# Optimization experiments

Hardware: AMD Instinct MI355X
Metric: run time of the kernel (lower is better)

## Reference

```python
import jax, jax.numpy as jnp
import numpy as np

B, T, D, R = 8, 4096, 768, 16
DB = D // 3  # bucket size (d_img = d_sym = 256, d_rf = D - 2*DB = 256)


def setup_inputs() -> dict:
    key = jax.random.key(0)
    ks = jax.random.split(key, 10)
    s = 0.05
    x = jax.random.normal(ks[0], (B, T, D), dtype=jnp.float32)
    # torch nn.Linear stores weight as (out, in); y = x @ W.T + b
    V_w = jax.random.normal(ks[1], (R, D), dtype=jnp.float32) * s
    U_w = jax.random.normal(ks[2], (D, R), dtype=jnp.float32) * s
    E1_w = jax.random.normal(ks[3], (DB, D), dtype=jnp.float32) * s
    E1_b = jnp.zeros((DB,), dtype=jnp.float32)
    E2_w = jax.random.normal(ks[4], (3, DB), dtype=jnp.float32) * s
    E2_b = jnp.zeros((3,), dtype=jnp.float32)
    # a_base init per bucket: img=-0.6, sym=-1.0, rf=-1.6; a_delta init 0 (perturbed so tanh path is exercised)
    a_base = jnp.concatenate([
        jnp.full((DB,), -0.6, dtype=jnp.float32),
        jnp.full((DB,), -1.0, dtype=jnp.float32),
        jnp.full((D - 2 * DB,), -1.6, dtype=jnp.float32),
    ])
    a_delta = jax.random.normal(ks[5], (D,), dtype=jnp.float32) * 0.1
    C_w = jax.random.normal(ks[6], (D, D), dtype=jnp.float32) * s
    G_w = jax.random.normal(ks[7], (D, D), dtype=jnp.float32) * s
    G_b = jnp.zeros((D,), dtype=jnp.float32)
    return {"x": x, "V_w": V_w, "U_w": U_w, "E1_w": E1_w, "E1_b": E1_b,
            "E2_w": E2_w, "E2_b": E2_b, "a_base": a_base, "a_delta": a_delta,
            "C_w": C_w, "G_w": G_w, "G_b": G_b}


def reference(x, V_w, U_w, E1_w, E1_b, E2_w, E2_b, a_base, a_delta, C_w, G_w, G_b):
    d = x.shape[-1]
    db = d // 3
    # Low-rank input projection: Bu = U(V(x))
    Z = jnp.einsum('btd,rd->btr', x, V_w)            # (B,T,R)
    Bu = jnp.einsum('btr,dr->btd', Z, U_w)           # (B,T,D)
    # Evidence scores per timestep (3 clinical buckets)
    h = jax.nn.gelu(jnp.einsum('btd,ed->bte', x, E1_w) + E1_b, approximate=False)
    alpha = jax.nn.sigmoid(jnp.einsum('bte,ce->btc', h, E2_w) + E2_b)  # (B,T,3)
    # Broadcast each bucket's evidence score over its channels
    alpha_rep = jnp.concatenate([
        jnp.broadcast_to(alpha[..., 0:1], alpha.shape[:-1] + (db,)),
        jnp.broadcast_to(alpha[..., 1:2], alpha.shape[:-1] + (db,)),
        jnp.broadcast_to(alpha[..., 2:3], alpha.shape[:-1] + (d - 2 * db,)),
    ], axis=-1)                                       # (B,T,D)
    a_eff = a_base + alpha_rep * jnp.tanh(a_delta)    # (B,T,D)
    lam = jnp.exp(-jax.nn.softplus(-a_eff))           # (B,T,D), in (0,1)
    # Diagonal linear recurrence s_t = lam_t * s_{t-1} + Bu_t  (scan over time)
    def step(s, inp):
        l_t, bu_t = inp
        s = l_t * s + bu_t
        return s, s
    s0 = jnp.zeros(x.shape[:1] + x.shape[2:], dtype=x.dtype)  # (B,D)
    _, S = jax.lax.scan(step, s0, (jnp.swapaxes(lam, 0, 1), jnp.swapaxes(Bu, 0, 1)))
    S = jnp.swapaxes(S, 0, 1)                         # (B,T,D)
    y = jnp.einsum('btd,od->bto', S, C_w)
    gate = jax.nn.sigmoid(jnp.einsum('btd,od->bto', x, G_w) + G_b)
    y = jax.nn.gelu(y, approximate=False) * gate
    return x + y  # dropout is identity in eval mode
```

## Files before the change

kernel.cpp:

```cpp
#include <hip/hip_runtime.h>
#include <hip/hip_bf16.h>
#include <math.h>

#define B_   8
#define T_   4096
#define D_   768
#define R_   16
#define DB_  256
#define N_   (B_ * T_)
#define NC_  64
#define L_   (T_ / NC_)
#define NKS_ (D_ / 32)

typedef __attribute__((ext_vector_type(8))) short bf16x8;
typedef __attribute__((ext_vector_type(4))) float f32x4;

__device__ __forceinline__ float gelu_exact(float x) {
    return 0.5f * x * (1.0f + erff(x * 0.70710678118654752f));
}
__device__ __forceinline__ float sigmoidf_(float x) {
    return 1.0f / (1.0f + expf(-x));
}
__device__ __forceinline__ float bf2f(unsigned short u) {
    return __uint_as_float(((unsigned)u) << 16);
}
__device__ __forceinline__ unsigned short f2bf(float f) {
    __hip_bfloat16 h = __float2bfloat16(f);
    return *(unsigned short*)&h;
}

__device__ __forceinline__ void gload16(const unsigned short* g, unsigned short* l) {
    __builtin_amdgcn_global_load_lds(
        (const __attribute__((address_space(1))) unsigned int*)(const void*)g,
        (__attribute__((address_space(3))) unsigned int*)(void*)l,
        16, 0, 0);
}

__device__ __forceinline__ void stage_tile(const unsigned short* src, int ld,
                                           int row0, int k0,
                                           unsigned short* lds, int w, int l) {
#pragma unroll
    for (int j = 0; j < 2; ++j) {
        int i   = ((w * 2 + j) << 6) + l;
        int row = i >> 2;
        int q   = i & 3;
        int qs  = q ^ ((row >> 1) & 3);
        const unsigned short* g = src + (size_t)(row0 + row) * ld + k0 + qs * 8;
        gload16(g, lds + ((w * 2 + j) << 9));
    }
}

__device__ __forceinline__ bf16x8 frag_read(const unsigned short* lds, int row, int lq) {
    int q = lq ^ ((row >> 1) & 3);
    return *(const bf16x8*)(lds + row * 32 + q * 8);
}

__device__ __forceinline__ void tile_mfma(const unsigned short* bc,
                                          int wrow, int wcol, int lr, int lq,
                                          f32x4 acc[4][4]) {
    bf16x8 a[4], b[4];
#pragma unroll
    for (int m = 0; m < 4; m++) a[m] = frag_read(bc, wrow + m * 16 + lr, lq);
#pragma unroll
    for (int n = 0; n < 4; n++) b[n] = frag_read(bc + 4096, wcol + n * 16 + lr, lq);
#pragma unroll
    for (int m = 0; m < 4; m++)
#pragma unroll
        for (int n = 0; n < 4; n++)
            acc[m][n] = __builtin_amdgcn_mfma_f32_16x16x32_bf16(a[m], b[n], acc[m][n], 0, 0, 0);
}

__device__ __forceinline__ void kloop3(const unsigned short* __restrict__ A,
                                       const unsigned short* __restrict__ Bm,
                                       int row0, int col0,
                                       unsigned short* lds,
                                       int w, int l, f32x4 acc[4][4]) {
    const int lr = l & 15, lq = l >> 4;
    const int wrow = (w >> 1) * 64, wcol = (w & 1) * 64;

    stage_tile(A,  D_, row0, 0,  lds,         w, l);
    stage_tile(Bm, D_, col0, 0,  lds + 4096,  w, l);
    stage_tile(A,  D_, row0, 32, lds + 8192,  w, l);
    stage_tile(Bm, D_, col0, 32, lds + 12288, w, l);

#pragma unroll 3
    for (int t = 0; t < NKS_ - 2; ++t) {
        asm volatile("s_waitcnt vmcnt(4)" ::: "memory");
        __builtin_amdgcn_s_barrier();
        __builtin_amdgcn_sched_barrier(0);
        unsigned short* bn = lds + ((t + 2) % 3) * 8192;
        stage_tile(A,  D_, row0, (t + 2) * 32, bn,        w, l);
        stage_tile(Bm, D_, col0, (t + 2) * 32, bn + 4096, w, l);
        tile_mfma(lds + (t % 3) * 8192, wrow, wcol, lr, lq, acc);
    }
    asm volatile("s_waitcnt vmcnt(4)" ::: "memory");
    __builtin_amdgcn_s_barrier();
    __builtin_amdgcn_sched_barrier(0);
    tile_mfma(lds + ((NKS_ - 2) % 3) * 8192, wrow, wcol, lr, lq, acc);
    asm volatile("s_waitcnt vmcnt(0)" ::: "memory");
    __builtin_amdgcn_s_barrier();
    __builtin_amdgcn_sched_barrier(0);
    tile_mfma(lds + ((NKS_ - 1) % 3) * 8192, wrow, wcol, lr, lq, acc);
}

__device__ __forceinline__ void tile_decode(int nwg, int ncol, int& rowt, int& colt) {
    int bid = blockIdx.x;
    int cpx = nwg >> 3;
    int swz = (bid & 7) * cpx + (bid >> 3);
    colt = swz % ncol;
    rowt = swz / ncol;
}

__global__ __launch_bounds__(256, 3)
void gemm_e1_mfma(const unsigned short* __restrict__ Xb,
                  const unsigned short* __restrict__ Wb,
                  const float* __restrict__ bias,
                  unsigned short* __restrict__ H) {
    __shared__ unsigned short lds[3 * 8192];
    const int t = threadIdx.x, l = t & 63, w = t >> 6;
    int rowt, colt;
    tile_decode(512, 2, rowt, colt);
    const int row0 = rowt * 128, col0 = colt * 128;
    const int lr = l & 15, lq = l >> 4;
    const int wrow = (w >> 1) * 64, wcol = (w & 1) * 64;
    f32x4 acc[4][4] = {};
    kloop3(Xb, Wb, row0, col0, lds, w, l, acc);
#pragma unroll
    for (int m = 0; m < 4; m++)
#pragma unroll
        for (int n = 0; n < 4; n++) {
            int col = col0 + wcol + n * 16 + lr;
            float bc = bias[col];
#pragma unroll
            for (int r = 0; r < 4; r++) {
                int row = row0 + wrow + m * 16 + lq * 4 + r;
                H[(size_t)row * DB_ + col] = f2bf(gelu_exact(acc[m][n][r] + bc));
            }
        }
}

__global__ __launch_bounds__(256, 3)
void gemm_fused_out(const unsigned short* __restrict__ Xb,
                    const unsigned short* __restrict__ Gwb,
                    const unsigned short* __restrict__ Sb,
                    const unsigned short* __restrict__ Cwb,
                    const float* __restrict__ Gbias,
                    const float* __restrict__ X32,
                    float* __restrict__ out) {
    __shared__ unsigned short lds[3 * 8192];
    const int t = threadIdx.x, l = t & 63, w = t >> 6;
    int rowt, colt;
    tile_decode(1536, 6, rowt, colt);
    const int row0 = rowt * 128, col0 = colt * 128;
    const int lr = l & 15, lq = l >> 4;
    const int wrow = (w >> 1) * 64, wcol = (w & 1) * 64;

    f32x4 acc[4][4] = {};
    kloop3(Xb, Gwb, row0, col0, lds, w, l, acc);

    unsigned int gp[4][4][2];
#pragma unroll
    for (int m = 0; m < 4; m++)
#pragma unroll
        for (int n = 0; n < 4; n++) {
            float gb = Gbias[col0 + wcol + n * 16 + lr];
            gp[m][n][0] = (unsigned)f2bf(sigmoidf_(acc[m][n][0] + gb))
                        | ((unsigned)f2bf(sigmoidf_(acc[m][n][1] + gb)) << 16);
            gp[m][n][1] = (unsigned)f2bf(sigmoidf_(acc[m][n][2] + gb))
                        | ((unsigned)f2bf(sigmoidf_(acc[m][n][3] + gb)) << 16);
            acc[m][n] = (f32x4){0.f, 0.f, 0.f, 0.f};
        }

    kloop3(Sb, Cwb, row0, col0, lds, w, l, acc);

#pragma unroll
    for (int m = 0; m < 4; m++)
#pragma unroll
        for (int n = 0; n < 4; n++) {
            int col = col0 + wcol + n * 16 + lr;
#pragma unroll
            for (int r = 0; r < 4; r++) {
                int row = row0 + wrow + m * 16 + lq * 4 + r;
                size_t o = (size_t)row * D_ + col;
                float g = bf2f((unsigned short)(gp[m][n][r >> 1] >> ((r & 1) * 16)));
                out[o] = X32[o] + gelu_exact(acc[m][n][r]) * g;
            }
        }
}

__global__ __launch_bounds__(256)
void z_mfma(const unsigned short* __restrict__ Xb,
            const unsigned short* __restrict__ Vb,
            float* __restrict__ Z) {
    const int t = threadIdx.x, l = t & 63, w = t >> 6;
    const int lr = l & 15, lq = l >> 4;
    const int tok0 = (blockIdx.x * 4 + w) * 16;
    f32x4 acc = {};
#pragma unroll
    for (int k0 = 0; k0 < D_; k0 += 32) {
        bf16x8 a = *(const bf16x8*)&Xb[(size_t)(tok0 + lr) * D_ + k0 + lq * 8];
        bf16x8 b = *(const bf16x8*)&Vb[(size_t)lr * D_ + k0 + lq * 8];
        acc = __builtin_amdgcn_mfma_f32_16x16x32_bf16(a, b, acc, 0, 0, 0);
    }
#pragma unroll
    for (int rr = 0; rr < 4; rr++)
        Z[(size_t)(tok0 + lq * 4 + rr) * R_ + lr] = acc[rr];
}

__global__ __launch_bounds__(256)
void alpha_kernel(const unsigned short* __restrict__ H,
                  const float* __restrict__ E2w, const float* __restrict__ E2b,
                  float* __restrict__ alpha) {
    const int t = threadIdx.x, l = t & 63, w = t >> 6;
    const size_t tok = blockIdx.x * 4 + w;
    ushort4 hv = *(const ushort4*)&H[tok * DB_ + l * 4];
    float h0 = bf2f(hv.x), h1 = bf2f(hv.y), h2 = bf2f(hv.z), h3 = bf2f(hv.w);
    float p[3];
#pragma unroll
    for (int c = 0; c < 3; c++) {
        float4 e = *(const float4*)&E2w[c * DB_ + l * 4];
        p[c] = h0 * e.x + h1 * e.y + h2 * e.z + h3 * e.w;
#pragma unroll
        for (int m = 32; m >= 1; m >>= 1) p[c] += __shfl_xor(p[c], m);
    }
    if (l == 0) {
        alpha[tok * 3 + 0] = sigmoidf_(p[0] + E2b[0]);
        alpha[tok * 3 + 1] = sigmoidf_(p[1] + E2b[1]);
        alpha[tok * 3 + 2] = sigmoidf_(p[2] + E2b[2]);
    }
}

__device__ __forceinline__ void load_chunk_lds(const float* __restrict__ Z,
                                               const float* __restrict__ alpha,
                                               int tok0, int t,
                                               float* Zs, float* als) {
#pragma unroll
    for (int i = t; i < L_ * R_ / 4; i += 192)
        *(float4*)&Zs[i * 4] = *(const float4*)&Z[(size_t)tok0 * R_ + i * 4];
    als[t] = alpha[(size_t)tok0 * 3 + t];
}

__device__ __forceinline__ float dot16(const float* zrow, const float4* u) {
    float4 z0 = *(const float4*)&zrow[0],  z1 = *(const float4*)&zrow[4];
    float4 z2 = *(const float4*)&zrow[8],  z3 = *(const float4*)&zrow[12];
    return z0.x*u[0].x + z0.y*u[0].y + z0.z*u[0].z + z0.w*u[0].w
         + z1.x*u[1].x + z1.y*u[1].y + z1.z*u[1].z + z1.w*u[1].w
         + z2.x*u[2].x + z2.y*u[2].y + z2.z*u[2].z + z2.w*u[2].w
         + z3.x*u[3].x + z3.y*u[3].y + z3.z*u[3].z + z3.w*u[3].w;
}

__global__ __launch_bounds__(192)
void scan_pass1(const float* __restrict__ Z, const float* __restrict__ alpha,
                const float* __restrict__ Uw, const float* __restrict__ a_base,
                const float* __restrict__ tanhd,
                float* __restrict__ Aagg, float* __restrict__ Send) {
    __shared__ float Zs[L_ * R_];
    __shared__ float als[L_ * 3];
    const int t = threadIdx.x;
    const int c = blockIdx.x & (NC_ - 1);
    const int b = blockIdx.x >> 6;
    const int tok0 = b * T_ + c * L_;
    const int d0 = t * 4;
    const int buck = d0 >> 8;
    load_chunk_lds(Z, alpha, tok0, t, Zs, als);

    float4 u[4][4];
#pragma unroll
    for (int j = 0; j < 4; j++)
#pragma unroll
        for (int q = 0; q < 4; q++)
            u[j][q] = *(const float4*)&Uw[(size_t)(d0 + j) * R_ + q * 4];
    float4 ab = *(const float4*)&a_base[d0];
    float4 td = *(const float4*)&tanhd[d0];
    float abv[4] = {ab.x, ab.y, ab.z, ab.w};
    float tdv[4] = {td.x, td.y, td.z, td.w};
    __syncthreads();

    float a[4] = {1.f, 1.f, 1.f, 1.f}, s[4] = {};
    for (int i = 0; i < L_; i++) {
        float av = als[i * 3 + buck];
#pragma unroll
        for (int j = 0; j < 4; j++) {
            float lam = sigmoidf_(fmaf(av, tdv[j], abv[j]));
            float bu  = dot16(&Zs[i * R_], u[j]);
            a[j] *= lam;
            s[j] = fmaf(lam, s[j], bu);
        }
    }
    size_t o = ((size_t)(b * NC_ + c)) * D_ + d0;
    *(float4*)&Aagg[o] = make_float4(a[0], a[1], a[2], a[3]);
    *(float4*)&Send[o] = make_float4(s[0], s[1], s[2], s[3]);
}

__global__ void scan_pass2(const float* __restrict__ Aagg, const float* __restrict__ Send,
                           float* __restrict__ Cin) {
    const int d = threadIdx.x;
    const int b = blockIdx.x;
    float s = 0.f;
    for (int c = 0; c < NC_; c++) {
        size_t o = ((size_t)(b * NC_ + c)) * D_ + d;
        Cin[o] = s;
        s = fmaf(Aagg[o], s, Send[o]);
    }
}

__global__ __launch_bounds__(192)
void scan_pass3(const float* __restrict__ Z, const float* __restrict__ alpha,
                const float* __restrict__ Uw, const float* __restrict__ a_base,
                const float* __restrict__ tanhd, const float* __restrict__ Cin,
                unsigned short* __restrict__ Sout) {
    __shared__ float Zs[L_ * R_];
    __shared__ float als[L_ * 3];
    const int t = threadIdx.x;
    const int c = blockIdx.x & (NC_ - 1);
    const int b = blockIdx.x >> 6;
    const int tok0 = b * T_ + c * L_;
    const int d0 = t * 4;
    const int buck = d0 >> 8;
    load_chunk_lds(Z, alpha, tok0, t, Zs, als);

    float4 u[4][4];
#pragma unroll
    for (int j = 0; j < 4; j++)
#pragma unroll
        for (int q = 0; q < 4; q++)
            u[j][q] = *(const float4*)&Uw[(size_t)(d0 + j) * R_ + q * 4];
    float4 ab = *(const float4*)&a_base[d0];
    float4 td = *(const float4*)&tanhd[d0];
    float abv[4] = {ab.x, ab.y, ab.z, ab.w};
    float tdv[4] = {td.x, td.y, td.z, td.w};
    __syncthreads();

    size_t ci = ((size_t)(b * NC_ + c)) * D_ + d0;
    float4 c4 = *(const float4*)&Cin[ci];
    float s[4] = {c4.x, c4.y, c4.z, c4.w};
    for (int i = 0; i < L_; i++) {
        float av = als[i * 3 + buck];
#pragma unroll
        for (int j = 0; j < 4; j++) {
            float lam = sigmoidf_(fmaf(av, tdv[j], abv[j]));
            float bu  = dot16(&Zs[i * R_], u[j]);
            s[j] = fmaf(lam, s[j], bu);
        }
        *(ushort4*)&Sout[(size_t)(tok0 + i) * D_ + d0] =
            make_ushort4(f2bf(s[0]), f2bf(s[1]), f2bf(s[2]), f2bf(s[3]));
    }
}

__global__ void cvt_bf16_vec(const float* __restrict__ in, unsigned short* __restrict__ out, int n4) {
    int i = blockIdx.x * 256 + threadIdx.x;
    if (i < n4) {
        float4 v = ((const float4*)in)[i];
        ((ushort4*)out)[i] = make_ushort4(f2bf(v.x), f2bf(v.y), f2bf(v.z), f2bf(v.w));
    }
}
__global__ void tanh_vec(const float* __restrict__ in, float* __restrict__ out, int n) {
    int i = blockIdx.x * 256 + threadIdx.x;
    if (i < n) out[i] = tanhf(in[i]);
}

extern "C" void kernel_launch(void* const* d_in, const int* in_sizes, int n_in,
                              void* d_out, int out_size, void* d_ws, size_t ws_size,
                              hipStream_t stream) {
    const float* x       = (const float*)d_in[0];
    const float* V_w     = (const float*)d_in[1];
    const float* U_w     = (const float*)d_in[2];
    const float* E1_w    = (const float*)d_in[3];
    const float* E1_b    = (const float*)d_in[4];
    const float* E2_w    = (const float*)d_in[5];
    const float* E2_b    = (const float*)d_in[6];
    const float* a_base  = (const float*)d_in[7];
    const float* a_delta = (const float*)d_in[8];
    const float* C_w     = (const float*)d_in[9];
    const float* G_w     = (const float*)d_in[10];
    const float* G_b     = (const float*)d_in[11];
    float* out = (float*)d_out;

    char* p = (char*)d_ws;
    float* Aagg  = (float*)p;           p += (size_t)B_ * NC_ * D_ * 4;
    float* Send  = (float*)p;           p += (size_t)B_ * NC_ * D_ * 4;
    float* Cin   = (float*)p;           p += (size_t)B_ * NC_ * D_ * 4;
    float* tanhd = (float*)p;           p += (size_t)D_ * 4;
    float* Z     = (float*)p;           p += (size_t)N_ * R_ * 4;
    float* alpha = (float*)p;           p += (size_t)N_ * 3 * 4;
    unsigned short* x_bf  = (unsigned short*)p; p += (size_t)N_ * D_ * 2;
    unsigned short* H_bf  = (unsigned short*)p; p += (size_t)N_ * DB_ * 2;
    unsigned short* S_bf  = (unsigned short*)p; p += (size_t)N_ * D_ * 2;
    unsigned short* E1_bf = (unsigned short*)p; p += (size_t)DB_ * D_ * 2;
    unsigned short* Cw_bf = (unsigned short*)p; p += (size_t)D_ * D_ * 2;
    unsigned short* Gw_bf = (unsigned short*)p; p += (size_t)D_ * D_ * 2;
    unsigned short* V_bf  = (unsigned short*)p; p += (size_t)R_ * D_ * 2;

    {
        int n4 = N_ * D_ / 4;
        cvt_bf16_vec<<<(n4 + 255) / 256, 256, 0, stream>>>(x, x_bf, n4);
        n4 = DB_ * D_ / 4;
        cvt_bf16_vec<<<(n4 + 255) / 256, 256, 0, stream>>>(E1_w, E1_bf, n4);
        n4 = D_ * D_ / 4;
        cvt_bf16_vec<<<(n4 + 255) / 256, 256, 0, stream>>>(C_w, Cw_bf, n4);
        cvt_bf16_vec<<<(n4 + 255) / 256, 256, 0, stream>>>(G_w, Gw_bf, n4);
        n4 = R_ * D_ / 4;
        cvt_bf16_vec<<<(n4 + 255) / 256, 256, 0, stream>>>(V_w, V_bf, n4);
        tanh_vec<<<3, 256, 0, stream>>>(a_delta, tanhd, D_);
    }

    gemm_e1_mfma<<<512, 256, 0, stream>>>(x_bf, E1_bf, E1_b, H_bf);
    alpha_kernel<<<N_ / 4, 256, 0, stream>>>(H_bf, E2_w, E2_b, alpha);
    z_mfma<<<N_ / 64, 256, 0, stream>>>(x_bf, V_bf, Z);

    scan_pass1<<<B_ * NC_, 192, 0, stream>>>(Z, alpha, U_w, a_base, tanhd, Aagg, Send);
    scan_pass2<<<B_,       D_,  0, stream>>>(Aagg, Send, Cin);
    scan_pass3<<<B_ * NC_, 192, 0, stream>>>(Z, alpha, U_w, a_base, tanhd, Cin, S_bf);

    gemm_fused_out<<<1536, 256, 0, stream>>>(x_bf, Gw_bf, S_bf, Cw_bf, G_b, x, out);
}
```

Baseline: 342.0 us.

## Fuse x conversion into Z projection, overlap out-GEMM prologue, use bf16 residual

Result: faster. 300.2 us (-12.2%).

```diff
diff --git a/kernel.cpp b/kernel.cpp
--- a/kernel.cpp
+++ b/kernel.cpp
@@ -28,6 +28,14 @@
     __hip_bfloat16 h = __float2bfloat16(f);
     return *(unsigned short*)&h;
 }
+__device__ __forceinline__ bf16x8 pack8(float4 a, float4 b) {
+    bf16x8 r;
+    r[0] = (short)f2bf(a.x); r[1] = (short)f2bf(a.y);
+    r[2] = (short)f2bf(a.z); r[3] = (short)f2bf(a.w);
+    r[4] = (short)f2bf(b.x); r[5] = (short)f2bf(b.y);
+    r[6] = (short)f2bf(b.z); r[7] = (short)f2bf(b.w);
+    return r;
+}
 
 __device__ __forceinline__ void gload16(const unsigned short* g, unsigned short* l) {
     __builtin_amdgcn_global_load_lds(
@@ -63,13 +71,26 @@
     for (int m = 0; m < 4; m++) a[m] = frag_read(bc, wrow + m * 16 + lr, lq);
 #pragma unroll
     for (int n = 0; n < 4; n++) b[n] = frag_read(bc + 4096, wcol + n * 16 + lr, lq);
+    __builtin_amdgcn_s_setprio(1);
 #pragma unroll
     for (int m = 0; m < 4; m++)
 #pragma unroll
         for (int n = 0; n < 4; n++)
             acc[m][n] = __builtin_amdgcn_mfma_f32_16x16x32_bf16(a[m], b[n], acc[m][n], 0, 0, 0);
-}
-
+    __builtin_amdgcn_s_setprio(0);
+}
+
+__device__ __forceinline__ void kloop_prologue(const unsigned short* __restrict__ A,
+                                               const unsigned short* __restrict__ Bm,
+                                               int row0, int col0,
+                                               unsigned short* lds, int w, int l) {
+    stage_tile(A,  D_, row0, 0,  lds,         w, l);
+    stage_tile(Bm, D_, col0, 0,  lds + 4096,  w, l);
+    stage_tile(A,  D_, row0, 32, lds + 8192,  w, l);
+    stage_tile(Bm, D_, col0, 32, lds + 12288, w, l);
+}
+
+template <bool DO_PROLOGUE>
 __device__ __forceinline__ void kloop3(const unsigned short* __restrict__ A,
                                        const unsigned short* __restrict__ Bm,
                                        int row0, int col0,
@@ -78,10 +99,7 @@
     const int lr = l & 15, lq = l >> 4;
     const int wrow = (w >> 1) * 64, wcol = (w & 1) * 64;
 
-    stage_tile(A,  D_, row0, 0,  lds,         w, l);
-    stage_tile(Bm, D_, col0, 0,  lds + 4096,  w, l);
-    stage_tile(A,  D_, row0, 32, lds + 8192,  w, l);
-    stage_tile(Bm, D_, col0, 32, lds + 12288, w, l);
+    if (DO_PROLOGUE) kloop_prologue(A, Bm, row0, col0, lds, w, l);
 
 #pragma unroll 3
     for (int t = 0; t < NKS_ - 2; ++t) {
@@ -124,7 +142,7 @@
     const int lr = l & 15, lq = l >> 4;
     const int wrow = (w >> 1) * 64, wcol = (w & 1) * 64;
     f32x4 acc[4][4] = {};
-    kloop3(Xb, Wb, row0, col0, lds, w, l, acc);
+    kloop3<true>(Xb, Wb, row0, col0, lds, w, l, acc);
 #pragma unroll
     for (int m = 0; m < 4; m++)
 #pragma unroll
@@ -145,7 +163,6 @@
                     const unsigned short* __restrict__ Sb,
                     const unsigned short* __restrict__ Cwb,
                     const float* __restrict__ Gbias,
-                    const float* __restrict__ X32,
                     float* __restrict__ out) {
     __shared__ unsigned short lds[3 * 8192];
     const int t = threadIdx.x, l = t & 63, w = t >> 6;
@@ -155,23 +172,28 @@
     const int lr = l & 15, lq = l >> 4;
     const int wrow = (w >> 1) * 64, wcol = (w & 1) * 64;
 
+    float gb[4];
+#pragma unroll
+    for (int n = 0; n < 4; n++) gb[n] = Gbias[col0 + wcol + n * 16 + lr];
+
     f32x4 acc[4][4] = {};
-    kloop3(Xb, Gwb, row0, col0, lds, w, l, acc);
+    kloop3<true>(Xb, Gwb, row0, col0, lds, w, l, acc);
+
+    kloop_prologue(Sb, Cwb, row0, col0, lds, w, l);
 
     unsigned int gp[4][4][2];
 #pragma unroll
     for (int m = 0; m < 4; m++)
 #pragma unroll
         for (int n = 0; n < 4; n++) {
-            float gb = Gbias[col0 + wcol + n * 16 + lr];
-            gp[m][n][0] = (unsigned)f2bf(sigmoidf_(acc[m][n][0] + gb))
-                        | ((unsigned)f2bf(sigmoidf_(acc[m][n][1] + gb)) << 16);
-            gp[m][n][1] = (unsigned)f2bf(sigmoidf_(acc[m][n][2] + gb))
-                        | ((unsigned)f2bf(sigmoidf_(acc[m][n][3] + gb)) << 16);
+            gp[m][n][0] = (unsigned)f2bf(sigmoidf_(acc[m][n][0] + gb[n]))
+                        | ((unsigned)f2bf(sigmoidf_(acc[m][n][1] + gb[n])) << 16);
+            gp[m][n][1] = (unsigned)f2bf(sigmoidf_(acc[m][n][2] + gb[n]))
+                        | ((unsigned)f2bf(sigmoidf_(acc[m][n][3] + gb[n])) << 16);
             acc[m][n] = (f32x4){0.f, 0.f, 0.f, 0.f};
         }
 
-    kloop3(Sb, Cwb, row0, col0, lds, w, l, acc);
+    kloop3<false>(Sb, Cwb, row0, col0, lds, w, l, acc);
 
 #pragma unroll
     for (int m = 0; m < 4; m++)
@@ -183,24 +205,31 @@
                 int row = row0 + wrow + m * 16 + lq * 4 + r;
                 size_t o = (size_t)row * D_ + col;
                 float g = bf2f((unsigned short)(gp[m][n][r >> 1] >> ((r & 1) * 16)));
-                out[o] = X32[o] + gelu_exact(acc[m][n][r]) * g;
+                out[o] = bf2f(Xb[o]) + gelu_exact(acc[m][n][r]) * g;
             }
         }
 }
 
 __global__ __launch_bounds__(256)
-void z_mfma(const unsigned short* __restrict__ Xb,
-            const unsigned short* __restrict__ Vb,
-            float* __restrict__ Z) {
+void cvtz_kernel(const float* __restrict__ X, const float* __restrict__ Vw,
+                 unsigned short* __restrict__ Xb, float* __restrict__ Z) {
     const int t = threadIdx.x, l = t & 63, w = t >> 6;
     const int lr = l & 15, lq = l >> 4;
     const int tok0 = (blockIdx.x * 4 + w) * 16;
+    const float* xrow = X  + (size_t)(tok0 + lr) * D_;
+    const float* vrow = Vw + (size_t)lr * D_;
     f32x4 acc = {};
-#pragma unroll
+#pragma unroll 4
     for (int k0 = 0; k0 < D_; k0 += 32) {
-        bf16x8 a = *(const bf16x8*)&Xb[(size_t)(tok0 + lr) * D_ + k0 + lq * 8];
-        bf16x8 b = *(const bf16x8*)&Vb[(size_t)lr * D_ + k0 + lq * 8];
-        acc = __builtin_amdgcn_mfma_f32_16x16x32_bf16(a, b, acc, 0, 0, 0);
+        int k = k0 + lq * 8;
+        float4 xa = *(const float4*)&xrow[k];
+        float4 xb = *(const float4*)&xrow[k + 4];
+        float4 va = *(const float4*)&vrow[k];
+        float4 vb = *(const float4*)&vrow[k + 4];
+        bf16x8 xf = pack8(xa, xb);
+        bf16x8 vf = pack8(va, vb);
+        *(bf16x8*)&Xb[(size_t)(tok0 + lr) * D_ + k] = xf;
+        acc = __builtin_amdgcn_mfma_f32_16x16x32_bf16(xf, vf, acc, 0, 0, 0);
     }
 #pragma unroll
     for (int rr = 0; rr < 4; rr++)
@@ -389,28 +418,24 @@
     unsigned short* E1_bf = (unsigned short*)p; p += (size_t)DB_ * D_ * 2;
     unsigned short* Cw_bf = (unsigned short*)p; p += (size_t)D_ * D_ * 2;
     unsigned short* Gw_bf = (unsigned short*)p; p += (size_t)D_ * D_ * 2;
-    unsigned short* V_bf  = (unsigned short*)p; p += (size_t)R_ * D_ * 2;
 
     {
-        int n4 = N_ * D_ / 4;
-        cvt_bf16_vec<<<(n4 + 255) / 256, 256, 0, stream>>>(x, x_bf, n4);
-        n4 = DB_ * D_ / 4;
+        int n4 = DB_ * D_ / 4;
         cvt_bf16_vec<<<(n4 + 255) / 256, 256, 0, stream>>>(E1_w, E1_bf, n4);
         n4 = D_ * D_ / 4;
         cvt_bf16_vec<<<(n4 + 255) / 256, 256, 0, stream>>>(C_w, Cw_bf, n4);
         cvt_bf16_vec<<<(n4 + 255) / 256, 256, 0, stream>>>(G_w, Gw_bf, n4);
-        n4 = R_ * D_ / 4;
-        cvt_bf16_vec<<<(n4 + 255) / 256, 256, 0, stream>>>(V_w, V_bf, n4);
         tanh_vec<<<3, 256, 0, stream>>>(a_delta, tanhd, D_);
     }
+
+    cvtz_kernel<<<N_ / 64, 256, 0, stream>>>(x, V_w, x_bf, Z);
 
     gemm_e1_mfma<<<512, 256, 0, stream>>>(x_bf, E1_bf, E1_b, H_bf);
     alpha_kernel<<<N_ / 4, 256, 0, stream>>>(H_bf, E2_w, E2_b, alpha);
-    z_mfma<<<N_ / 64, 256, 0, stream>>>(x_bf, V_bf, Z);
 
     scan_pass1<<<B_ * NC_, 192, 0, stream>>>(Z, alpha, U_w, a_base, tanhd, Aagg, Send);
     scan_pass2<<<B_,       D_,  0, stream>>>(Aagg, Send, Cin);
     scan_pass3<<<B_ * NC_, 192, 0, stream>>>(Z, alpha, U_w, a_base, tanhd, Cin, S_bf);
 
-    gemm_fused_out<<<1536, 256, 0, stream>>>(x_bf, Gw_bf, S_bf, Cw_bf, G_b, x, out);
-}
+    gemm_fused_out<<<1536, 256, 0, stream>>>(x_bf, Gw_bf, S_bf, Cw_bf, G_b, out);
+}
```
